# Kernel optimization log

Hardware: AMD Instinct MI355X
Metric: run time of the kernel (lower is better)

Reference implementation:

```python
import jax, jax.numpy as jnp
import numpy as np

EPS = 1e-12  # tf.math.l2_normalize default epsilon

def _l2_normalize(x, axis):
    sq = jnp.sum(x * x, axis=axis, keepdims=True)
    return x * jax.lax.rsqrt(jnp.maximum(sq, EPS))

def setup_inputs() -> dict:
    key = jax.random.key(0)
    k1, k2 = jax.random.split(key)
    B, L, D, K = 4096, 200, 64, 8
    inputs = jax.random.normal(k1, (B, L, D), dtype=jnp.float32)
    prototype = jax.random.normal(k2, (K, D), dtype=jnp.float32)
    return {"inputs": inputs, "prototype": prototype}

def reference(inputs, prototype):
    # inputs: [B, L, D], prototype: [K, D]
    normed_interests = _l2_normalize(inputs, axis=-1)      # [B, L, D]
    normed_prototype = _l2_normalize(prototype, axis=-1)   # [K, D]
    # cosine_sim: [B, K, L] = prototype @ interests^T (broadcast over batch)
    cosine_sim = jnp.einsum('kd,bld->bkl', normed_prototype, normed_interests)
    # softmax over the slot/prototype axis K (axis=-2)
    attn = jax.nn.softmax(cosine_sim, axis=-2)              # [B, K, L]
    # projected interests: [B, K, D]
    return jnp.einsum('bkl,bld->bkd', attn, inputs)
```

## Files before the change

kernel.cpp:

```cpp
#include <hip/hip_runtime.h>


#define LQ 200
#define DQ 64
#define KQ 8
#define NSTEP 25

typedef float v2f __attribute__((ext_vector_type(2)));

__device__ __forceinline__ float dppx1(float v) {
    return __int_as_float(__builtin_amdgcn_update_dpp(0, __float_as_int(v), 0xB1, 0xF, 0xF, true));
}
__device__ __forceinline__ float dppx2(float v) {
    return __int_as_float(__builtin_amdgcn_update_dpp(0, __float_as_int(v), 0x4E, 0xF, 0xF, true));
}
__device__ __forceinline__ float swz4(float v) {
    return __int_as_float(__builtin_amdgcn_ds_swizzle(__float_as_int(v), 0x101F));
}
__device__ __forceinline__ float allred8(float v) {
    v += dppx1(v); v += dppx2(v); v += swz4(v); return v;
}
__device__ __forceinline__ v2f fma2(v2f a, v2f b, v2f c) {
    return __builtin_elementwise_fma(a, b, c);
}
__device__ __forceinline__ float hsum2(v2f v) { return v.x + v.y; }

__device__ __forceinline__ float reduce_dots(const float* s, bool b1, bool b2, bool b3) {
    float T0 = (b1 ? s[1] : s[0]) + dppx1(b1 ? s[0] : s[1]);
    float T1 = (b1 ? s[3] : s[2]) + dppx1(b1 ? s[2] : s[3]);
    float T2 = (b1 ? s[5] : s[4]) + dppx1(b1 ? s[4] : s[5]);
    float T3 = (b1 ? s[7] : s[6]) + dppx1(b1 ? s[6] : s[7]);
    float K0 = (b2 ? T1 : T0) + dppx2(b2 ? T0 : T1);
    float K1 = (b2 ? T3 : T2) + dppx2(b2 ? T2 : T3);
    return (b3 ? K1 : K0) + swz4(b3 ? K0 : K1);
}

__global__ __launch_bounds__(64) void projector_kernel(const float* __restrict__ x,
                                                       const float* __restrict__ proto,
                                                       float* __restrict__ out) {
    const int b = blockIdx.x;
    const int t = threadIdx.x;
    const int c = t & 7;
    const int a = t >> 3;
    const bool b1 = (c & 1) != 0;
    const bool b2 = (c & 2) != 0;
    const bool b3 = (c & 4) != 0;

    const float4* p4  = (const float4*)proto;
    const float4* xb4 = (const float4*)(x + (size_t)b * (LQ * DQ));

    float4 pA[KQ], pB[KQ];
    #pragma unroll
    for (int k = 0; k < KQ; ++k) {
        pA[k] = p4[k * 16 + 2 * c];
        pB[k] = p4[k * 16 + 2 * c + 1];
    }
    float rnp;
    {
        float sp[KQ];
        #pragma unroll
        for (int k = 0; k < KQ; ++k) {
            v2f a0 = {pA[k].x, pA[k].y}, a1 = {pA[k].z, pA[k].w};
            v2f b0 = {pB[k].x, pB[k].y}, b1v = {pB[k].z, pB[k].w};
            v2f t2 = fma2(b1v, b1v, fma2(b0, b0, fma2(a1, a1, a0 * a0)));
            sp[k] = hsum2(t2);
        }
        rnp = __builtin_amdgcn_rsqf(fmaxf(reduce_dots(sp, b1, b2, b3), 1e-12f));
    }

    v2f acc[KQ][4];
    #pragma unroll
    for (int j = 0; j < KQ; ++j)
        #pragma unroll
        for (int q = 0; q < 4; ++q) acc[j][q] = (v2f){0.f, 0.f};

    float4 f0 = xb4[a * 16 + 2 * c], f1 = xb4[a * 16 + 2 * c + 1];

    #pragma unroll 1
    for (int it = 0; it < NSTEP; ++it) {
        const int nrow = (it + 1 < NSTEP ? (it + 1) * 8 : (NSTEP - 1) * 8) + a;
        float4 nf0 = xb4[nrow * 16 + 2 * c];
        float4 nf1 = xb4[nrow * 16 + 2 * c + 1];

        v2f x0 = {f0.x, f0.y}, x1 = {f0.z, f0.w};
        v2f x2 = {f1.x, f1.y}, x3 = {f1.z, f1.w};

        float s[KQ];
        #pragma unroll
        for (int k = 0; k < KQ; ++k) {
            v2f pa0 = {pA[k].x, pA[k].y}, pa1 = {pA[k].z, pA[k].w};
            v2f pb0 = {pB[k].x, pB[k].y}, pb1 = {pB[k].z, pB[k].w};
            v2f t2 = fma2(x3, pb1, fma2(x2, pb0, fma2(x1, pa1, x0 * pa0)));
            s[k] = hsum2(t2);
        }
        float d = reduce_dots(s, b1, b2, b3) * rnp;

        v2f q2 = fma2(x3, x3, fma2(x2, x2, fma2(x1, x1, x0 * x0)));
        float sq = allred8(hsum2(q2));

        float e0 = __expf(d * __builtin_amdgcn_rsqf(fmaxf(sq, 1e-12f)));
        float e1 = dppx1(e0);
        float e2 = dppx2(e0);
        float e3 = dppx2(e1);
        float e4 = swz4(e0);
        float e5 = swz4(e1);
        float e6 = swz4(e2);
        float e7 = swz4(e3);
        float rd = __builtin_amdgcn_rcpf(((e0 + e1) + (e2 + e3)) + ((e4 + e5) + (e6 + e7)));
        float aj[KQ] = {e0 * rd, e1 * rd, e2 * rd, e3 * rd,
                        e4 * rd, e5 * rd, e6 * rd, e7 * rd};

        #pragma unroll
        for (int j = 0; j < KQ; ++j) {
            v2f aa = {aj[j], aj[j]};
            acc[j][0] = fma2(aa, x0, acc[j][0]);
            acc[j][1] = fma2(aa, x1, acc[j][1]);
            acc[j][2] = fma2(aa, x2, acc[j][2]);
            acc[j][3] = fma2(aa, x3, acc[j][3]);
        }

        f0 = nf0; f1 = nf1;
    }

    #pragma unroll
    for (int i = 0; i < 4; ++i)
        #pragma unroll
        for (int q = 0; q < 4; ++q) {
            v2f send = (a & 1) ? acc[i][q] : acc[i + 4][q];
            v2f keep = (a & 1) ? acc[i + 4][q] : acc[i][q];
            v2f r = {__shfl_xor(send.x, 8, 64), __shfl_xor(send.y, 8, 64)};
            acc[i][q] = keep + r;
        }
    #pragma unroll
    for (int i = 0; i < 2; ++i)
        #pragma unroll
        for (int q = 0; q < 4; ++q) {
            v2f send = (a & 2) ? acc[i][q] : acc[i + 2][q];
            v2f keep = (a & 2) ? acc[i + 2][q] : acc[i][q];
            v2f r = {__shfl_xor(send.x, 16, 64), __shfl_xor(send.y, 16, 64)};
            acc[i][q] = keep + r;
        }
    #pragma unroll
    for (int q = 0; q < 4; ++q) {
        v2f send = (a & 4) ? acc[0][q] : acc[1][q];
        v2f keep = (a & 4) ? acc[1][q] : acc[0][q];
        v2f r = {__shfl_xor(send.x, 32, 64), __shfl_xor(send.y, 32, 64)};
        acc[0][q] = keep + r;
    }

    const int j = ((a & 1) << 2) | (a & 2) | ((a & 4) >> 2);
    const int k = c ^ j;
    float4* og = (float4*)(out + (size_t)b * (KQ * DQ));
    og[k * 16 + 2 * c]     = make_float4(acc[0][0].x, acc[0][0].y, acc[0][1].x, acc[0][1].y);
    og[k * 16 + 2 * c + 1] = make_float4(acc[0][2].x, acc[0][2].y, acc[0][3].x, acc[0][3].y);
}

extern "C" void kernel_launch(void* const* d_in, const int* in_sizes, int n_in,
                              void* d_out, int out_size, void* d_ws, size_t ws_size,
                              hipStream_t stream) {
    const float* x     = (const float*)d_in[0];
    const float* proto = (const float*)d_in[1];
    float* out = (float*)d_out;

    const int Bn = in_sizes[0] / (LQ * DQ);

    projector_kernel<<<Bn, 64, 0, stream>>>(x, proto, out);
}
```

Measured before the change: 44.38 us.

## Deepen global-load prefetch to four steps and replace swizzle with DPP row xor

The per-batch loop now keeps four steps of input rows in flight in registers, unrolled by four, instead of a single-step prefetch. This is meant to hide global memory latency better when only one 64-thread block handles each batch. The ds_swizzle xor-4 exchange is replaced by two DPP row_shl/row_shr moves with bank masks, avoiding the LDS-path swizzle latency. A launch_bounds minimum-blocks hint of 2 is also added. Together these raise register pressure, which could lower occupancy or cause spills.

```diff
diff --git a/kernel.cpp b/kernel.cpp
--- a/kernel.cpp
+++ b/kernel.cpp
@@ -14,11 +14,14 @@
 __device__ __forceinline__ float dppx2(float v) {
     return __int_as_float(__builtin_amdgcn_update_dpp(0, __float_as_int(v), 0x4E, 0xF, 0xF, true));
 }
-__device__ __forceinline__ float swz4(float v) {
-    return __int_as_float(__builtin_amdgcn_ds_swizzle(__float_as_int(v), 0x101F));
+__device__ __forceinline__ float xor4(float v) {
+    int vi = __float_as_int(v);
+    int r1 = __builtin_amdgcn_update_dpp(0,  vi, 0x104, 0xF, 0x5, false);
+    int r  = __builtin_amdgcn_update_dpp(r1, vi, 0x114, 0xF, 0xA, false);
+    return __int_as_float(r);
 }
 __device__ __forceinline__ float allred8(float v) {
-    v += dppx1(v); v += dppx2(v); v += swz4(v); return v;
+    v += dppx1(v); v += dppx2(v); v += xor4(v); return v;
 }
 __device__ __forceinline__ v2f fma2(v2f a, v2f b, v2f c) {
     return __builtin_elementwise_fma(a, b, c);
@@ -32,40 +35,85 @@
     float T3 = (b1 ? s[7] : s[6]) + dppx1(b1 ? s[6] : s[7]);
     float K0 = (b2 ? T1 : T0) + dppx2(b2 ? T0 : T1);
     float K1 = (b2 ? T3 : T2) + dppx2(b2 ? T2 : T3);
-    return (b3 ? K1 : K0) + swz4(b3 ? K0 : K1);
-}
-
-__global__ __launch_bounds__(64) void projector_kernel(const float* __restrict__ x,
-                                                       const float* __restrict__ proto,
-                                                       float* __restrict__ out) {
+    return (b3 ? K1 : K0) + xor4(b3 ? K0 : K1);
+}
+
+struct Ctx {
+    float4 pA[KQ], pB[KQ];
+    float rnp;
+    bool b1, b2, b3;
+};
+
+__device__ __forceinline__ void step_compute(float4 f0, float4 f1,
+                                             const Ctx& cx, v2f (&acc)[KQ][4]) {
+    v2f x0 = {f0.x, f0.y}, x1 = {f0.z, f0.w};
+    v2f x2 = {f1.x, f1.y}, x3 = {f1.z, f1.w};
+
+    float s[KQ];
+    #pragma unroll
+    for (int k = 0; k < KQ; ++k) {
+        v2f pa0 = {cx.pA[k].x, cx.pA[k].y}, pa1 = {cx.pA[k].z, cx.pA[k].w};
+        v2f pb0 = {cx.pB[k].x, cx.pB[k].y}, pb1 = {cx.pB[k].z, cx.pB[k].w};
+        v2f t2 = fma2(x3, pb1, fma2(x2, pb0, fma2(x1, pa1, x0 * pa0)));
+        s[k] = hsum2(t2);
+    }
+    float d = reduce_dots(s, cx.b1, cx.b2, cx.b3) * cx.rnp;
+
+    v2f q2 = fma2(x3, x3, fma2(x2, x2, fma2(x1, x1, x0 * x0)));
+    float sq = allred8(hsum2(q2));
+
+    float e0 = __expf(d * __builtin_amdgcn_rsqf(fmaxf(sq, 1e-12f)));
+    float e1 = dppx1(e0);
+    float e2 = dppx2(e0);
+    float e3 = dppx2(e1);
+    float e4 = xor4(e0);
+    float e5 = xor4(e1);
+    float e6 = xor4(e2);
+    float e7 = xor4(e3);
+    float rd = __builtin_amdgcn_rcpf(((e0 + e1) + (e2 + e3)) + ((e4 + e5) + (e6 + e7)));
+    float aj[KQ] = {e0 * rd, e1 * rd, e2 * rd, e3 * rd,
+                    e4 * rd, e5 * rd, e6 * rd, e7 * rd};
+
+    #pragma unroll
+    for (int j = 0; j < KQ; ++j) {
+        v2f aa = {aj[j], aj[j]};
+        acc[j][0] = fma2(aa, x0, acc[j][0]);
+        acc[j][1] = fma2(aa, x1, acc[j][1]);
+        acc[j][2] = fma2(aa, x2, acc[j][2]);
+        acc[j][3] = fma2(aa, x3, acc[j][3]);
+    }
+}
+
+__global__ __launch_bounds__(64, 2) void projector_kernel(const float* __restrict__ x,
+                                                          const float* __restrict__ proto,
+                                                          float* __restrict__ out) {
     const int b = blockIdx.x;
     const int t = threadIdx.x;
     const int c = t & 7;
     const int a = t >> 3;
-    const bool b1 = (c & 1) != 0;
-    const bool b2 = (c & 2) != 0;
-    const bool b3 = (c & 4) != 0;
+
+    Ctx cx;
+    cx.b1 = (c & 1) != 0;
+    cx.b2 = (c & 2) != 0;
+    cx.b3 = (c & 4) != 0;
 
     const float4* p4  = (const float4*)proto;
     const float4* xb4 = (const float4*)(x + (size_t)b * (LQ * DQ));
 
-    float4 pA[KQ], pB[KQ];
     #pragma unroll
     for (int k = 0; k < KQ; ++k) {
-        pA[k] = p4[k * 16 + 2 * c];
-        pB[k] = p4[k * 16 + 2 * c + 1];
-    }
-    float rnp;
+        cx.pA[k] = p4[k * 16 + 2 * c];
+        cx.pB[k] = p4[k * 16 + 2 * c + 1];
+    }
     {
         float sp[KQ];
         #pragma unroll
         for (int k = 0; k < KQ; ++k) {
-            v2f a0 = {pA[k].x, pA[k].y}, a1 = {pA[k].z, pA[k].w};
-            v2f b0 = {pB[k].x, pB[k].y}, b1v = {pB[k].z, pB[k].w};
-            v2f t2 = fma2(b1v, b1v, fma2(b0, b0, fma2(a1, a1, a0 * a0)));
-            sp[k] = hsum2(t2);
-        }
-        rnp = __builtin_amdgcn_rsqf(fmaxf(reduce_dots(sp, b1, b2, b3), 1e-12f));
+            v2f a0 = {cx.pA[k].x, cx.pA[k].y}, a1 = {cx.pA[k].z, cx.pA[k].w};
+            v2f b0 = {cx.pB[k].x, cx.pB[k].y}, b1v = {cx.pB[k].z, cx.pB[k].w};
+            sp[k] = hsum2(fma2(b1v, b1v, fma2(b0, b0, fma2(a1, a1, a0 * a0))));
+        }
+        cx.rnp = __builtin_amdgcn_rsqf(fmaxf(reduce_dots(sp, cx.b1, cx.b2, cx.b3), 1e-12f));
     }
 
     v2f acc[KQ][4];
@@ -74,53 +122,42 @@
         #pragma unroll
         for (int q = 0; q < 4; ++q) acc[j][q] = (v2f){0.f, 0.f};
 
-    float4 f0 = xb4[a * 16 + 2 * c], f1 = xb4[a * 16 + 2 * c + 1];
+    const int lofs = a * 16 + 2 * c;
+
+    float4 s0a = xb4[0 * 128 + lofs], s0b = xb4[0 * 128 + lofs + 1];
+    float4 s1a = xb4[1 * 128 + lofs], s1b = xb4[1 * 128 + lofs + 1];
+    float4 s2a = xb4[2 * 128 + lofs], s2b = xb4[2 * 128 + lofs + 1];
+    float4 s3a = xb4[3 * 128 + lofs], s3b = xb4[3 * 128 + lofs + 1];
 
     #pragma unroll 1
-    for (int it = 0; it < NSTEP; ++it) {
-        const int nrow = (it + 1 < NSTEP ? (it + 1) * 8 : (NSTEP - 1) * 8) + a;
-        float4 nf0 = xb4[nrow * 16 + 2 * c];
-        float4 nf1 = xb4[nrow * 16 + 2 * c + 1];
-
-        v2f x0 = {f0.x, f0.y}, x1 = {f0.z, f0.w};
-        v2f x2 = {f1.x, f1.y}, x3 = {f1.z, f1.w};
-
-        float s[KQ];
-        #pragma unroll
-        for (int k = 0; k < KQ; ++k) {
-            v2f pa0 = {pA[k].x, pA[k].y}, pa1 = {pA[k].z, pA[k].w};
-            v2f pb0 = {pB[k].x, pB[k].y}, pb1 = {pB[k].z, pB[k].w};
-            v2f t2 = fma2(x3, pb1, fma2(x2, pb0, fma2(x1, pa1, x0 * pa0)));
-            s[k] = hsum2(t2);
-        }
-        float d = reduce_dots(s, b1, b2, b3) * rnp;
-
-        v2f q2 = fma2(x3, x3, fma2(x2, x2, fma2(x1, x1, x0 * x0)));
-        float sq = allred8(hsum2(q2));
-
-        float e0 = __expf(d * __builtin_amdgcn_rsqf(fmaxf(sq, 1e-12f)));
-        float e1 = dppx1(e0);
-        float e2 = dppx2(e0);
-        float e3 = dppx2(e1);
-        float e4 = swz4(e0);
-        float e5 = swz4(e1);
-        float e6 = swz4(e2);
-        float e7 = swz4(e3);
-        float rd = __builtin_amdgcn_rcpf(((e0 + e1) + (e2 + e3)) + ((e4 + e5) + (e6 + e7)));
-        float aj[KQ] = {e0 * rd, e1 * rd, e2 * rd, e3 * rd,
-                        e4 * rd, e5 * rd, e6 * rd, e7 * rd};
-
-        #pragma unroll
-        for (int j = 0; j < KQ; ++j) {
-            v2f aa = {aj[j], aj[j]};
-            acc[j][0] = fma2(aa, x0, acc[j][0]);
-            acc[j][1] = fma2(aa, x1, acc[j][1]);
-            acc[j][2] = fma2(aa, x2, acc[j][2]);
-            acc[j][3] = fma2(aa, x3, acc[j][3]);
-        }
-
-        f0 = nf0; f1 = nf1;
-    }
+    for (int g = 0; g < 6; ++g) {
+        const int base = 4 * g;
+        {
+            const int sn = (base + 4 < NSTEP) ? base + 4 : NSTEP - 1;
+            float4 na = xb4[sn * 128 + lofs], nb = xb4[sn * 128 + lofs + 1];
+            step_compute(s0a, s0b, cx, acc);
+            s0a = na; s0b = nb;
+        }
+        {
+            const int sn = (base + 5 < NSTEP) ? base + 5 : NSTEP - 1;
+            float4 na = xb4[sn * 128 + lofs], nb = xb4[sn * 128 + lofs + 1];
+            step_compute(s1a, s1b, cx, acc);
+            s1a = na; s1b = nb;
+        }
+        {
+            const int sn = (base + 6 < NSTEP) ? base + 6 : NSTEP - 1;
+            float4 na = xb4[sn * 128 + lofs], nb = xb4[sn * 128 + lofs + 1];
+            step_compute(s2a, s2b, cx, acc);
+            s2a = na; s2b = nb;
+        }
+        {
+            const int sn = (base + 7 < NSTEP) ? base + 7 : NSTEP - 1;
+            float4 na = xb4[sn * 128 + lofs], nb = xb4[sn * 128 + lofs + 1];
+            step_compute(s3a, s3b, cx, acc);
+            s3a = na; s3b = nb;
+        }
+    }
+    step_compute(s0a, s0b, cx, acc);
 
     #pragma unroll
     for (int i = 0; i < 4; ++i)
```

Measured after the change: 43.54 us. No clear change (-1.9%).
